# Performance work log

Hardware: AMD Instinct MI355X
Metric: run time of the kernel (lower is better)

The kernel has to match this reference:

```python
import jax, jax.numpy as jnp
import numpy as np

D_MODEL = 1024
NUM_HEADS = 16
HEAD_DIM = D_MODEL // NUM_HEADS


def setup_inputs() -> dict:
    key = jax.random.key(0)
    ks = jax.random.split(key, 9)
    s = 1.0 / np.sqrt(D_MODEL)
    inp = {
        "x": jax.random.normal(ks[0], (4, 2048, D_MODEL), dtype=jnp.float32),
        "wq": jax.random.uniform(ks[1], (D_MODEL, D_MODEL), jnp.float32, -s, s),
        "bq": jax.random.uniform(ks[2], (D_MODEL,), jnp.float32, -s, s),
        "wk": jax.random.uniform(ks[3], (D_MODEL, D_MODEL), jnp.float32, -s, s),
        "bk": jax.random.uniform(ks[4], (D_MODEL,), jnp.float32, -s, s),
        "wv": jax.random.uniform(ks[5], (D_MODEL, D_MODEL), jnp.float32, -s, s),
        "bv": jax.random.uniform(ks[6], (D_MODEL,), jnp.float32, -s, s),
        "wo": jax.random.uniform(ks[7], (D_MODEL, D_MODEL), jnp.float32, -s, s),
        "bo": jax.random.uniform(ks[8], (D_MODEL,), jnp.float32, -s, s),
    }
    return inp


def _split_heads(t):
    # [B, S, D] -> [B, H, S, Dh]
    b, s, _ = t.shape
    return t.reshape(b, s, NUM_HEADS, HEAD_DIM).transpose(0, 2, 1, 3)


def reference(x, wq, bq, wk, bk, wv, bv, wo, bo):
    b, s, _ = x.shape
    q = _split_heads(x @ wq.T + bq)
    k = _split_heads(x @ wk.T + bk)
    v = _split_heads(x @ wv.T + bv)
    scale = 1.0 / np.sqrt(HEAD_DIM).astype(np.float32)
    scores = jnp.einsum('bhqd,bhkd->bhqk', q, k) * scale  # [B,H,S,S]
    probs = jax.nn.softmax(scores, axis=-1)
    ctx = jnp.einsum('bhqk,bhkd->bhqd', probs, v)  # [B,H,S,Dh]
    ctx = ctx.transpose(0, 2, 1, 3).reshape(b, s, D_MODEL)
    return ctx @ wo.T + bo
```

## Files before the change

kernel.cpp:

```cpp
#include <hip/hip_runtime.h>
#include <stdint.h>

typedef short bf16x8 __attribute__((ext_vector_type(8)));
typedef float f32x4 __attribute__((ext_vector_type(4)));

#define D_MODEL 1024
#define NHEAD   16
#define HDIM    64
#define BATCH   4
#define SEQ     2048
#define NTOK    (BATCH * SEQ)

#define BM 128
#define BN 128
#define BK 64

#define LOG2E 1.44269504088896340736f

__device__ __forceinline__ unsigned short f2bf_fast(float f) {
  return (unsigned short)((__float_as_uint(f) + 0x8000u) >> 16);
}

__device__ __forceinline__ void gload_lds16(const unsigned short* g, unsigned short* l) {
  __builtin_amdgcn_global_load_lds((const __attribute__((address_space(1))) void*)g,
                                   (__attribute__((address_space(3))) void*)l,
                                   16, 0, 0);
}

__global__ __launch_bounds__(256) void cvt_all(
    const float* __restrict__ x, const float* __restrict__ wq,
    const float* __restrict__ wk, const float* __restrict__ wv,
    const float* __restrict__ wo, unsigned short* __restrict__ dst) {
  long i = ((long)blockIdx.x * 256 + threadIdx.x) * 4;
  const float* src; long off;
  if (i < 8388608)       { src = x;  off = 0; }
  else if (i < 9437184)  { src = wq; off = 8388608; }
  else if (i < 10485760) { src = wk; off = 9437184; }
  else if (i < 11534336) { src = wv; off = 10485760; }
  else                   { src = wo; off = 11534336; }
  const float4 v = *(const float4*)(src + (i - off));
  ushort4 o = make_ushort4(f2bf_fast(v.x), f2bf_fast(v.y), f2bf_fast(v.z), f2bf_fast(v.w));
  *(ushort4*)(dst + i) = o;
}

__device__ __forceinline__ void gemm_bt_mainloop(
    const unsigned short* __restrict__ Abase,
    const unsigned short* __restrict__ Bbase,
    int lda, int ldb, int K,
    unsigned short* sA, unsigned short* sB,
    f32x4 acc[4][4]) {
  const int tid = threadIdx.x;
  const int wave = tid >> 6, lane = tid & 63;
  const int ln15 = lane & 15, quad = lane >> 4;
  const int wy = wave >> 1, wx = wave & 1;

#pragma unroll
  for (int mt = 0; mt < 4; ++mt)
#pragma unroll
    for (int nt = 0; nt < 4; ++nt)
      acc[mt][nt] = (f32x4){0.f, 0.f, 0.f, 0.f};

  for (int k0 = 0; k0 < K; k0 += BK) {
    __syncthreads();
#pragma unroll
    for (int i = 0; i < 4; ++i) {
      int chunk = i * 256 + wave * 64 + lane;
      int row = chunk >> 3, c = (chunk & 7) ^ (row & 7);
      gload_lds16(Abase + row * lda + k0 + c * 8, sA + (i * 256 + wave * 64) * 8);
      gload_lds16(Bbase + row * ldb + k0 + c * 8, sB + (i * 256 + wave * 64) * 8);
    }
    __syncthreads();
#pragma unroll
    for (int ks = 0; ks < 2; ++ks) {
      const int swz = ((ks * 4 + quad) ^ (ln15 & 7)) * 8;
      bf16x8 af[4], bfv[4];
#pragma unroll
      for (int t = 0; t < 4; ++t)
        af[t] = *(const bf16x8*)(sA + (64 * wy + 16 * t + ln15) * BK + swz);
#pragma unroll
      for (int t = 0; t < 4; ++t)
        bfv[t] = *(const bf16x8*)(sB + (64 * wx + 16 * t + ln15) * BK + swz);
#pragma unroll
      for (int mt = 0; mt < 4; ++mt)
#pragma unroll
        for (int nt = 0; nt < 4; ++nt)
          acc[mt][nt] = __builtin_amdgcn_mfma_f32_16x16x32_bf16(af[mt], bfv[nt], acc[mt][nt], 0, 0, 0);
    }
  }
}

#define TSTR 136
__global__ __launch_bounds__(256) void qkv_gemm(
    const unsigned short* __restrict__ xb,
    const unsigned short* __restrict__ wqb, const unsigned short* __restrict__ wkb,
    const unsigned short* __restrict__ wvb,
    const float* __restrict__ bq, const float* __restrict__ bk, const float* __restrict__ bv,
    unsigned short* __restrict__ Qb, unsigned short* __restrict__ Kb,
    unsigned short* __restrict__ Vt) {
  const int z = blockIdx.z;
  const unsigned short* W = (z == 0) ? wqb : (z == 1) ? wkb : wvb;
  const float* bias = (z == 0) ? bq : (z == 1) ? bk : bv;
  const int m0 = blockIdx.x * BM, n0 = blockIdx.y * BN;

  __shared__ __align__(16) unsigned char smem[BM * TSTR * 2];
  unsigned short* sA = (unsigned short*)smem;
  unsigned short* sB = (unsigned short*)(smem + BM * BK * 2);
  unsigned short* sT = (unsigned short*)smem;

  f32x4 acc[4][4];
  gemm_bt_mainloop(xb + (size_t)m0 * D_MODEL, W + (size_t)n0 * D_MODEL,
                   D_MODEL, D_MODEL, D_MODEL, sA, sB, acc);

  const int tid = threadIdx.x;
  const int lane = tid & 63, wave = tid >> 6;
  const int ln15 = lane & 15, quad = lane >> 4;
  const int wy = wave >> 1, wx = wave & 1;
  const int b = m0 >> 11;

  if (z == 2) {
    __syncthreads();
#pragma unroll
    for (int mt = 0; mt < 4; ++mt)
#pragma unroll
      for (int nt = 0; nt < 4; ++nt) {
        int j = 64 * wx + 16 * nt + ln15;
        float bj = bias[n0 + j];
#pragma unroll
        for (int r = 0; r < 4; r += 2) {
          int tok = 64 * wy + 16 * mt + quad * 4 + r;
          unsigned int pk = (unsigned int)f2bf_fast(acc[mt][nt][r] + bj) |
                            ((unsigned int)f2bf_fast(acc[mt][nt][r + 1] + bj) << 16);
          *(unsigned int*)(sT + j * TSTR + tok) = pk;
        }
      }
    __syncthreads();
    const int sbase = (m0 & 2047) + (tid & 15) * 8;
#pragma unroll
    for (int i = 0; i < 8; ++i) {
      int j = (tid >> 4) + i * 16;
      int feature = n0 + j;
      int h = feature >> 6, d = feature & 63;
      bf16x8 val = *(const bf16x8*)(sT + j * TSTR + (tid & 15) * 8);
      *(bf16x8*)(Vt + (((size_t)(b * NHEAD + h)) * HDIM + d) * SEQ + sbase) = val;
    }
  } else {
    const float scale = (z == 0) ? 0.125f * LOG2E : 1.0f;
    unsigned short* dst = (z == 0) ? Qb : Kb;
    __syncthreads();
    float bj[4];
#pragma unroll
    for (int nt = 0; nt < 4; ++nt) bj[nt] = bias[n0 + 64 * wx + 16 * nt + ln15];
#pragma unroll
    for (int mt = 0; mt < 4; ++mt)
#pragma unroll
      for (int nt = 0; nt < 4; ++nt)
#pragma unroll
        for (int r = 0; r < 4; ++r) {
          int tok = 64 * wy + 16 * mt + quad * 4 + r;
          int j = 64 * wx + 16 * nt + ln15;
          sT[tok * TSTR + j] = f2bf_fast((acc[mt][nt][r] + bj[nt]) * scale);
        }
    __syncthreads();
    const int srow = m0 & 2047;
#pragma unroll
    for (int i = 0; i < 8; ++i) {
      int tok = (tid >> 4) + i * 16;
      int jj = (tid & 15) * 8;
      bf16x8 val = *(const bf16x8*)(sT + tok * TSTR + jj);
      int feature = n0 + jj;
      int h = feature >> 6, d = feature & 63;
      *(bf16x8*)(dst + (((size_t)(b * NHEAD + h)) * SEQ + srow + tok) * HDIM + d) = val;
    }
  }
}

#define PSTR 72
__global__ __launch_bounds__(256, 4) void attn_kernel(
    const unsigned short* __restrict__ Qb,
    const unsigned short* __restrict__ Kb,
    const unsigned short* __restrict__ Vt,
    unsigned short* __restrict__ ctxb) {
  const int qb = blockIdx.x;
  const int bh = blockIdx.y;
  const int s0 = qb * 128;
  const int tid = threadIdx.x, wave = tid >> 6, lane = tid & 63;
  const int ln15 = lane & 15, quad = lane >> 4;

  __shared__ __align__(16) unsigned short sK[64 * 64], sV[64 * 64], sP[128 * PSTR];

  const unsigned short* Qg = Qb + (size_t)bh * SEQ * HDIM;
  const unsigned short* Kg = Kb + (size_t)bh * SEQ * HDIM;
  const unsigned short* Vg = Vt + (size_t)bh * HDIM * SEQ;

  bf16x8 qf[2][2];
#pragma unroll
  for (int mt = 0; mt < 2; ++mt)
#pragma unroll
    for (int ks = 0; ks < 2; ++ks)
      qf[mt][ks] = *(const bf16x8*)(Qg + (s0 + 32 * wave + 16 * mt + ln15) * HDIM + ks * 32 + quad * 8);

  const int chunk0 = wave * 64 + lane;
  const int row0 = chunk0 >> 3, c0 = (chunk0 & 7) ^ (row0 & 7);
  const int chunk1 = 256 + wave * 64 + lane;
  const int row1 = chunk1 >> 3, c1 = (chunk1 & 7) ^ (row1 & 7);
  const unsigned short* Kp0 = Kg + row0 * HDIM + c0 * 8;
  const unsigned short* Kp1 = Kg + row1 * HDIM + c1 * 8;
  const unsigned short* Vp0 = Vg + row0 * SEQ + c0 * 8;
  const unsigned short* Vp1 = Vg + row1 * SEQ + c1 * 8;
  unsigned short* dK0 = sK + chunk0 * 8;
  unsigned short* dK1 = sK + chunk1 * 8;
  unsigned short* dV0 = sV + chunk0 * 8;
  unsigned short* dV1 = sV + chunk1 * 8;

  unsigned short* sPw = sP + (32 * wave + 4 * quad) * PSTR + ln15;

  float l_part[8];
  f32x4 O[2][4];
#pragma unroll
  for (int i = 0; i < 8; ++i) l_part[i] = 0.f;
#pragma unroll
  for (int mt = 0; mt < 2; ++mt)
#pragma unroll
    for (int dt = 0; dt < 4; ++dt) O[mt][dt] = (f32x4){0.f, 0.f, 0.f, 0.f};

  for (int k0 = 0; k0 < SEQ; k0 += 64) {
    __syncthreads();
    gload_lds16(Kp0 + k0 * HDIM, dK0);
    gload_lds16(Kp1 + k0 * HDIM, dK1);
    gload_lds16(Vp0 + k0, dV0);
    gload_lds16(Vp1 + k0, dV1);
    __syncthreads();

    f32x4 sc[2][4];
#pragma unroll
    for (int mt = 0; mt < 2; ++mt)
#pragma unroll
      for (int nt = 0; nt < 4; ++nt) sc[mt][nt] = (f32x4){0.f, 0.f, 0.f, 0.f};
#pragma unroll
    for (int ks = 0; ks < 2; ++ks) {
      const int swz = ((ks * 4 + quad) ^ (ln15 & 7)) * 8;
#pragma unroll
      for (int nt = 0; nt < 4; ++nt) {
        bf16x8 bk8 = *(const bf16x8*)(sK + (16 * nt + ln15) * 64 + swz);
#pragma unroll
        for (int mt = 0; mt < 2; ++mt)
          sc[mt][nt] = __builtin_amdgcn_mfma_f32_16x16x32_bf16(qf[mt][ks], bk8, sc[mt][nt], 0, 0, 0);
      }
    }

#pragma unroll
    for (int mt = 0; mt < 2; ++mt)
#pragma unroll
      for (int r = 0; r < 4; ++r) {
        float p0 = __builtin_amdgcn_exp2f(sc[mt][0][r]);
        float p1 = __builtin_amdgcn_exp2f(sc[mt][1][r]);
        float p2 = __builtin_amdgcn_exp2f(sc[mt][2][r]);
        float p3 = __builtin_amdgcn_exp2f(sc[mt][3][r]);
        l_part[mt * 4 + r] += (p0 + p1) + (p2 + p3);
        unsigned short* pw = sPw + (16 * mt + r) * PSTR;
        pw[0]  = (unsigned short)((__float_as_uint(p0) + 0x8000u) >> 16);
        pw[16] = (unsigned short)((__float_as_uint(p1) + 0x8000u) >> 16);
        pw[32] = (unsigned short)((__float_as_uint(p2) + 0x8000u) >> 16);
        pw[48] = (unsigned short)((__float_as_uint(p3) + 0x8000u) >> 16);
      }

#pragma unroll
    for (int ks = 0; ks < 2; ++ks) {
      const int swz = ((ks * 4 + quad) ^ (ln15 & 7)) * 8;
      bf16x8 ap[2];
#pragma unroll
      for (int mt = 0; mt < 2; ++mt)
        ap[mt] = *(const bf16x8*)(sP + (32 * wave + 16 * mt + ln15) * PSTR + ks * 32 + quad * 8);
#pragma unroll
      for (int dt = 0; dt < 4; ++dt) {
        bf16x8 bv8 = *(const bf16x8*)(sV + (16 * dt + ln15) * 64 + swz);
#pragma unroll
        for (int mt = 0; mt < 2; ++mt)
          O[mt][dt] = __builtin_amdgcn_mfma_f32_16x16x32_bf16(ap[mt], bv8, O[mt][dt], 0, 0, 0);
      }
    }
  }

  const int b = bh >> 4, h = bh & 15;
#pragma unroll
  for (int mt = 0; mt < 2; ++mt)
#pragma unroll
    for (int r = 0; r < 4; ++r) {
      float l = l_part[mt * 4 + r];
      l += __shfl_xor(l, 1);
      l += __shfl_xor(l, 2);
      l += __shfl_xor(l, 4);
      l += __shfl_xor(l, 8);
      float inv = 1.0f / l;
      int token = b * SEQ + s0 + 32 * wave + 16 * mt + quad * 4 + r;
#pragma unroll
      for (int dt = 0; dt < 4; ++dt)
        ctxb[(size_t)token * D_MODEL + h * HDIM + 16 * dt + ln15] = f2bf_fast(O[mt][dt][r] * inv);
    }
}

__global__ __launch_bounds__(256) void oproj_kernel(
    const unsigned short* __restrict__ ctxb,
    const unsigned short* __restrict__ wob,
    const float* __restrict__ bo,
    float* __restrict__ out) {
  const int m0 = blockIdx.x * BM, n0 = blockIdx.y * BN;
  __shared__ __align__(16) unsigned short sA[BM * BK], sB[BN * BK];
  f32x4 acc[4][4];
  gemm_bt_mainloop(ctxb + (size_t)m0 * D_MODEL, wob + (size_t)n0 * D_MODEL,
                   D_MODEL, D_MODEL, D_MODEL, sA, sB, acc);

  const int lane = threadIdx.x & 63, wave = threadIdx.x >> 6;
  const int ln15 = lane & 15, quad = lane >> 4;
  const int wy = wave >> 1, wx = wave & 1;
#pragma unroll
  for (int mt = 0; mt < 4; ++mt)
#pragma unroll
    for (int nt = 0; nt < 4; ++nt)
#pragma unroll
      for (int r = 0; r < 4; ++r) {
        int n = m0 + 64 * wy + 16 * mt + quad * 4 + r;
        int j = n0 + 64 * wx + 16 * nt + ln15;
        out[(size_t)n * D_MODEL + j] = acc[mt][nt][r] + bo[j];
      }
}

extern "C" void kernel_launch(void* const* d_in, const int* in_sizes, int n_in,
                              void* d_out, int out_size, void* d_ws, size_t ws_size,
                              hipStream_t stream) {
  const float* x  = (const float*)d_in[0];
  const float* wq = (const float*)d_in[1];
  const float* bq = (const float*)d_in[2];
  const float* wk = (const float*)d_in[3];
  const float* bk = (const float*)d_in[4];
  const float* wv = (const float*)d_in[5];
  const float* bv = (const float*)d_in[6];
  const float* wo = (const float*)d_in[7];
  const float* bo = (const float*)d_in[8];
  float* out = (float*)d_out;

  unsigned short* ws   = (unsigned short*)d_ws;
  unsigned short* xb   = ws;
  unsigned short* wqb  = ws + 8388608;
  unsigned short* wkb  = ws + 9437184;
  unsigned short* wvb  = ws + 10485760;
  unsigned short* wob  = ws + 11534336;
  unsigned short* Qb   = ws + 12582912;
  unsigned short* Kb   = ws + 20971520;
  unsigned short* Vtb  = ws + 29360128;
  unsigned short* ctxb = ws + 37748736;

  cvt_all<<<12288, 256, 0, stream>>>(x, wq, wk, wv, wo, ws);

  qkv_gemm<<<dim3(64, 8, 3), 256, 0, stream>>>(xb, wqb, wkb, wvb, bq, bk, bv, Qb, Kb, Vtb);
  attn_kernel<<<dim3(16, 64), 256, 0, stream>>>(Qb, Kb, Vtb, ctxb);
  oproj_kernel<<<dim3(64, 8), 256, 0, stream>>>(ctxb, wob, bo, out);
}
```

Baseline: 279.0 us.

## Load K fragments directly to registers and double-buffer V tiles in attention

The attention kernel now reads K fragments straight from global memory into registers and double-buffers the V tile in LDS. The next V tile is prefetched while the current one is used, which removes one of the two barriers per iteration. The QKV GEMM folds the three weight matrices into one flattened 2D grid over contiguous weights, shrinks its shared tile stride, and adds an occupancy hint to launch bounds. The risk is uncoalesced global K loads with higher register pressure, and the transposed-V epilogue now has less LDS, since TSTR went from 136 to 128.

```diff
diff --git a/kernel.cpp b/kernel.cpp
--- a/kernel.cpp
+++ b/kernel.cpp
@@ -89,26 +89,26 @@
   }
 }
 
-#define TSTR 136
-__global__ __launch_bounds__(256) void qkv_gemm(
+#define TSTR 128
+__global__ __launch_bounds__(256, 5) void qkv_gemm(
     const unsigned short* __restrict__ xb,
-    const unsigned short* __restrict__ wqb, const unsigned short* __restrict__ wkb,
-    const unsigned short* __restrict__ wvb,
+    const unsigned short* __restrict__ wall,
     const float* __restrict__ bq, const float* __restrict__ bk, const float* __restrict__ bv,
     unsigned short* __restrict__ Qb, unsigned short* __restrict__ Kb,
     unsigned short* __restrict__ Vt) {
-  const int z = blockIdx.z;
-  const unsigned short* W = (z == 0) ? wqb : (z == 1) ? wkb : wvb;
+  const int n0g = blockIdx.y * BN;
+  const int z = n0g >> 10;
+  const int n0 = n0g & 1023;
   const float* bias = (z == 0) ? bq : (z == 1) ? bk : bv;
-  const int m0 = blockIdx.x * BM, n0 = blockIdx.y * BN;
-
-  __shared__ __align__(16) unsigned char smem[BM * TSTR * 2];
-  unsigned short* sA = (unsigned short*)smem;
-  unsigned short* sB = (unsigned short*)(smem + BM * BK * 2);
-  unsigned short* sT = (unsigned short*)smem;
+  const int m0 = blockIdx.x * BM;
+
+  __shared__ __align__(16) unsigned short smem[BM * BK + BN * BK];
+  unsigned short* sA = smem;
+  unsigned short* sB = smem + BM * BK;
+  unsigned short* sT = smem;
 
   f32x4 acc[4][4];
-  gemm_bt_mainloop(xb + (size_t)m0 * D_MODEL, W + (size_t)n0 * D_MODEL,
+  gemm_bt_mainloop(xb + (size_t)m0 * D_MODEL, wall + (size_t)n0g * D_MODEL,
                    D_MODEL, D_MODEL, D_MODEL, sA, sB, acc);
 
   const int tid = threadIdx.x;
@@ -186,7 +186,8 @@
   const int tid = threadIdx.x, wave = tid >> 6, lane = tid & 63;
   const int ln15 = lane & 15, quad = lane >> 4;
 
-  __shared__ __align__(16) unsigned short sK[64 * 64], sV[64 * 64], sP[128 * PSTR];
+  __shared__ __align__(16) unsigned short sV[2][64 * 64];
+  __shared__ __align__(16) unsigned short sP[128 * PSTR];
 
   const unsigned short* Qg = Qb + (size_t)bh * SEQ * HDIM;
   const unsigned short* Kg = Kb + (size_t)bh * SEQ * HDIM;
@@ -199,18 +200,17 @@
     for (int ks = 0; ks < 2; ++ks)
       qf[mt][ks] = *(const bf16x8*)(Qg + (s0 + 32 * wave + 16 * mt + ln15) * HDIM + ks * 32 + quad * 8);
 
-  const int chunk0 = wave * 64 + lane;
+  const unsigned short* kp[4];
+#pragma unroll
+  for (int nt = 0; nt < 4; ++nt)
+    kp[nt] = Kg + (16 * nt + ln15) * HDIM + quad * 8;
+
+  const int chunk0 = tid;
   const int row0 = chunk0 >> 3, c0 = (chunk0 & 7) ^ (row0 & 7);
-  const int chunk1 = 256 + wave * 64 + lane;
+  const int chunk1 = 256 + tid;
   const int row1 = chunk1 >> 3, c1 = (chunk1 & 7) ^ (row1 & 7);
-  const unsigned short* Kp0 = Kg + row0 * HDIM + c0 * 8;
-  const unsigned short* Kp1 = Kg + row1 * HDIM + c1 * 8;
   const unsigned short* Vp0 = Vg + row0 * SEQ + c0 * 8;
   const unsigned short* Vp1 = Vg + row1 * SEQ + c1 * 8;
-  unsigned short* dK0 = sK + chunk0 * 8;
-  unsigned short* dK1 = sK + chunk1 * 8;
-  unsigned short* dV0 = sV + chunk0 * 8;
-  unsigned short* dV1 = sV + chunk1 * 8;
 
   unsigned short* sPw = sP + (32 * wave + 4 * quad) * PSTR + ln15;
 
@@ -223,13 +223,25 @@
 #pragma unroll
     for (int dt = 0; dt < 4; ++dt) O[mt][dt] = (f32x4){0.f, 0.f, 0.f, 0.f};
 
-  for (int k0 = 0; k0 < SEQ; k0 += 64) {
-    __syncthreads();
-    gload_lds16(Kp0 + k0 * HDIM, dK0);
-    gload_lds16(Kp1 + k0 * HDIM, dK1);
-    gload_lds16(Vp0 + k0, dV0);
-    gload_lds16(Vp1 + k0, dV1);
-    __syncthreads();
+  gload_lds16(Vp0, &sV[0][chunk0 * 8]);
+  gload_lds16(Vp1, &sV[0][chunk1 * 8]);
+
+  for (int t = 0; t < 32; ++t) {
+    __syncthreads();
+
+    bf16x8 kf[4][2];
+#pragma unroll
+    for (int nt = 0; nt < 4; ++nt) {
+      kf[nt][0] = *(const bf16x8*)(kp[nt]);
+      kf[nt][1] = *(const bf16x8*)(kp[nt] + 32);
+      kp[nt] += 64 * HDIM;
+    }
+
+    if (t < 31) {
+      const int kn = (t + 1) * 64;
+      gload_lds16(Vp0 + kn, &sV[(t + 1) & 1][chunk0 * 8]);
+      gload_lds16(Vp1 + kn, &sV[(t + 1) & 1][chunk1 * 8]);
+    }
 
     f32x4 sc[2][4];
 #pragma unroll
@@ -237,16 +249,12 @@
 #pragma unroll
       for (int nt = 0; nt < 4; ++nt) sc[mt][nt] = (f32x4){0.f, 0.f, 0.f, 0.f};
 #pragma unroll
-    for (int ks = 0; ks < 2; ++ks) {
-      const int swz = ((ks * 4 + quad) ^ (ln15 & 7)) * 8;
-#pragma unroll
-      for (int nt = 0; nt < 4; ++nt) {
-        bf16x8 bk8 = *(const bf16x8*)(sK + (16 * nt + ln15) * 64 + swz);
+    for (int ks = 0; ks < 2; ++ks)
+#pragma unroll
+      for (int nt = 0; nt < 4; ++nt)
 #pragma unroll
         for (int mt = 0; mt < 2; ++mt)
-          sc[mt][nt] = __builtin_amdgcn_mfma_f32_16x16x32_bf16(qf[mt][ks], bk8, sc[mt][nt], 0, 0, 0);
-      }
-    }
+          sc[mt][nt] = __builtin_amdgcn_mfma_f32_16x16x32_bf16(qf[mt][ks], kf[nt][ks], sc[mt][nt], 0, 0, 0);
 
 #pragma unroll
     for (int mt = 0; mt < 2; ++mt)
@@ -264,6 +272,7 @@
         pw[48] = (unsigned short)((__float_as_uint(p3) + 0x8000u) >> 16);
       }
 
+    const unsigned short* sVc = sV[t & 1];
 #pragma unroll
     for (int ks = 0; ks < 2; ++ks) {
       const int swz = ((ks * 4 + quad) ^ (ln15 & 7)) * 8;
@@ -273,7 +282,7 @@
         ap[mt] = *(const bf16x8*)(sP + (32 * wave + 16 * mt + ln15) * PSTR + ks * 32 + quad * 8);
 #pragma unroll
       for (int dt = 0; dt < 4; ++dt) {
-        bf16x8 bv8 = *(const bf16x8*)(sV + (16 * dt + ln15) * 64 + swz);
+        bf16x8 bv8 = *(const bf16x8*)(sVc + (16 * dt + ln15) * 64 + swz);
 #pragma unroll
         for (int mt = 0; mt < 2; ++mt)
           O[mt][dt] = __builtin_amdgcn_mfma_f32_16x16x32_bf16(ap[mt], bv8, O[mt][dt], 0, 0, 0);
@@ -341,9 +350,7 @@
 
   unsigned short* ws   = (unsigned short*)d_ws;
   unsigned short* xb   = ws;
-  unsigned short* wqb  = ws + 8388608;
-  unsigned short* wkb  = ws + 9437184;
-  unsigned short* wvb  = ws + 10485760;
+  unsigned short* wall = ws + 8388608;
   unsigned short* wob  = ws + 11534336;
   unsigned short* Qb   = ws + 12582912;
   unsigned short* Kb   = ws + 20971520;
@@ -352,7 +359,7 @@
 
   cvt_all<<<12288, 256, 0, stream>>>(x, wq, wk, wv, wo, ws);
 
-  qkv_gemm<<<dim3(64, 8, 3), 256, 0, stream>>>(xb, wqb, wkb, wvb, bq, bk, bv, Qb, Kb, Vtb);
+  qkv_gemm<<<dim3(64, 24), 256, 0, stream>>>(xb, wall, bq, bk, bv, Qb, Kb, Vtb);
   attn_kernel<<<dim3(16, 64), 256, 0, stream>>>(Qb, Kb, Vtb, ctxb);
   oproj_kernel<<<dim3(64, 8), 256, 0, stream>>>(ctxb, wob, bo, out);
 }
```

After: 361.9 us. 29.7% more time.
